# Optimization experiments

Measured on AMD Instinct MI355X. Metric: run time of the kernel, lower is better.

Reference implementation:

```python
import jax, jax.numpy as jnp
import numpy as np

D_MODEL = 1024
B, S = 4, 2048


def setup_inputs() -> dict:
    key = jax.random.key(0)
    kx, km, kq, kk, kv, ko = jax.random.split(key, 6)
    x = jax.random.normal(kx, (B, S, D_MODEL), dtype=jnp.float32)
    mask = jax.random.randint(km, (B, S, S), 0, 2).astype(jnp.bool_)
    # flax Dense default kernel init: lecun_normal-ish; plain scaled normal is fine for a reference
    init_scale = 1.0 / np.sqrt(D_MODEL)
    Wq = jax.random.normal(kq, (D_MODEL, D_MODEL), dtype=jnp.float32) * init_scale
    Wk = jax.random.normal(kk, (D_MODEL, D_MODEL), dtype=jnp.float32) * init_scale
    Wv = jax.random.normal(kv, (D_MODEL, D_MODEL), dtype=jnp.float32) * init_scale
    Wo = jax.random.normal(ko, (D_MODEL, D_MODEL), dtype=jnp.float32) * init_scale
    return {"x": x, "mask": mask, "Wq": Wq, "Wk": Wk, "Wv": Wv, "Wo": Wo}


def reference(x, mask, Wq, Wk, Wv, Wo):
    # QKV projections (use_bias=False)
    q = jnp.einsum('bsd,de->bse', x, Wq)
    k = jnp.einsum('bsd,de->bse', x, Wk)
    v = jnp.einsum('bsd,de->bse', x, Wv)
    scale = jnp.sqrt(jnp.asarray(q.shape[-1], x.dtype)).astype(x.dtype)
    # [B, S, S] attention scores
    attn_scores = jnp.einsum('bqd,bkd->bqk', q, k) / scale
    attn_scores = jnp.where(mask, attn_scores, jnp.asarray(-1e10, x.dtype))
    attn_weights = jax.nn.softmax(attn_scores, axis=-1)
    attn_output = jnp.einsum('bqk,bkd->bqd', attn_weights, v)
    return jnp.einsum('bsd,de->bse', attn_output, Wo)
```

## Files before the change

### kernel.cpp

```cpp
#include <hip/hip_runtime.h>


#define DM 1024
#define SQ 2048
#define NB 4
typedef unsigned short U16;
typedef unsigned long long U64;
typedef short bhalf8 __attribute__((ext_vector_type(8)));
typedef float f32x4 __attribute__((ext_vector_type(4)));

__device__ inline U16 f2bf(float f) {
  unsigned int u = __float_as_uint(f);
  u += 0x7FFFu + ((u >> 16) & 1u);
  return (U16)(u >> 16);
}
__device__ inline float2 bfp2(unsigned int u) {
  float2 r;
  r.x = __uint_as_float(u << 16);
  r.y = __uint_as_float(u & 0xffff0000u);
  return r;
}
__device__ inline unsigned int packbf(float a, float b) {
  return (unsigned int)f2bf(a) | ((unsigned int)f2bf(b) << 16);
}

__device__ __forceinline__ void gload16(const U16* g, const U16* l) {
  unsigned int m0v =
      (unsigned int)__builtin_amdgcn_readfirstlane((int)(unsigned long long)l);
  asm volatile("s_mov_b32 m0, %0\n\t"
               "global_load_lds_dwordx4 %1, off"
               :
               : "s"(m0v), "v"(g)
               : "memory");
}

__global__ __launch_bounds__(256) void conv_f32_bf16(
    const float* __restrict__ src, U16* __restrict__ dst, float* __restrict__ rs) {
  int idx = blockIdx.x * 256 + threadIdx.x;
  if (idx < NB * SQ) rs[idx] = 0.f;
  int i = idx * 8;
  float4 a = *(const float4*)(src + i);
  float4 b = *(const float4*)(src + i + 4);
  uint4 w;
  w.x = packbf(a.x, a.y); w.y = packbf(a.z, a.w);
  w.z = packbf(b.x, b.y); w.w = packbf(b.z, b.w);
  *(uint4*)(dst + i) = w;
}

__global__ __launch_bounds__(256) void pack_mask(
    const int* __restrict__ mask, U64* __restrict__ pm) {
  const int lane = threadIdx.x & 63;
  const int wv = (blockIdx.x * 256 + threadIdx.x) >> 6;
#pragma unroll 4
  for (int i = 0; i < 32; ++i) {
    size_t g = (size_t)wv * 32 + i;
    int mk = mask[g * 64 + lane];
    U64 b = __ballot(mk != 0);
    if (lane == 0) pm[g] = b;
  }
}

__device__ inline void ldcvt16(const float* p, U16* d) {
#pragma unroll
  for (int i = 0; i < 4; ++i) {
    float4 f = *(const float4*)(p + i * 4);
    d[i * 4 + 0] = f2bf(f.x); d[i * 4 + 1] = f2bf(f.y);
    d[i * 4 + 2] = f2bf(f.z); d[i * 4 + 3] = f2bf(f.w);
  }
}
__device__ inline void ldcvt16(const U16* p, U16* d) {
  uint4 a = *(const uint4*)p;
  uint4 b = *(const uint4*)(p + 8);
  *(uint4*)d = a;
  *(uint4*)(d + 8) = b;
}

__global__ __launch_bounds__(256) void transp_w4(
    const float* __restrict__ Wq, const float* __restrict__ Wk,
    const float* __restrict__ Wo, const float* __restrict__ Wv,
    U16* __restrict__ WT, U16* __restrict__ WoT, U16* __restrict__ Wv16) {
  __shared__ U16 tile[64][72];
  const int z = blockIdx.z;
  const int r0 = blockIdx.y * 64, c0 = blockIdx.x * 64;
  const int t = threadIdx.x;
  const int tr = t >> 2, tc = (t & 3) * 16;
  if (z == 3) {
    U16 vals[16];
    ldcvt16(Wv + (size_t)(r0 + tr) * DM + c0 + tc, vals);
    U16* op = Wv16 + (size_t)(r0 + tr) * DM + c0 + tc;
    *(uint4*)op = *(uint4*)&vals[0];
    *(uint4*)(op + 8) = *(uint4*)&vals[8];
    return;
  }
  const float* src = (z == 0) ? Wq : (z == 1) ? Wk : Wo;
  U16* d = (z == 2) ? WoT : WT + (size_t)z * DM * DM;
  ldcvt16(src + (size_t)(r0 + tr) * DM + c0 + tc, &tile[tr][tc]);
  __syncthreads();
  U16 vals[16];
#pragma unroll
  for (int m = 0; m < 16; ++m) vals[m] = tile[tc + m][tr];
  U16* op = d + (size_t)(c0 + tr) * DM + r0 + tc;
  *(uint4*)op = *(uint4*)&vals[0];
  *(uint4*)(op + 8) = *(uint4*)&vals[8];
}

__global__ __launch_bounds__(256) void transp_bf16(
    const U16* __restrict__ src, U16* __restrict__ dst, int R, int C) {
  __shared__ U16 tile[64][72];
  const int z = blockIdx.z;
  src += (size_t)z * R * C;
  dst += (size_t)z * R * C;
  const int r0 = blockIdx.y * 64, c0 = blockIdx.x * 64;
  const int t = threadIdx.x;
  const int tr = t >> 2, tc = (t & 3) * 16;
  ldcvt16(src + (size_t)(r0 + tr) * C + c0 + tc, &tile[tr][tc]);
  __syncthreads();
  U16 vals[16];
#pragma unroll
  for (int m = 0; m < 16; ++m) vals[m] = tile[tc + m][tr];
  U16* op = dst + (size_t)(c0 + tr) * R + r0 + tc;
  *(uint4*)op = *(uint4*)&vals[0];
  *(uint4*)(op + 8) = *(uint4*)&vals[8];
}

template <int EP>
__global__ __launch_bounds__(256) void gemm_mfma(
    const U16* __restrict__ A, const U16* __restrict__ B, void* __restrict__ Cv,
    int M, int N, int K, long long sA, long long sB, long long sC,
    const int* __restrict__ mask, float* __restrict__ rowsum, float scale) {
  __shared__ U16 As[128 * 72];
  __shared__ U16 Bs[128 * 72];
  const int t = threadIdx.x;
  const int lane = t & 63, wave = t >> 6;
  const int wm = wave >> 1, wn = wave & 1;
  const int q = lane >> 4, ln = lane & 15;
  const int z = blockIdx.z;
  const int m0 = blockIdx.y * 128, n0 = blockIdx.x * 128;
  A += (size_t)z * sA;
  B += (size_t)z * sB;

  f32x4 acc[4][4] = {};

  const int srow = t >> 3;
  const int scol = (t & 7) * 8;

  for (int k0 = 0; k0 < K; k0 += 64) {
    const U16* ga = A + (size_t)(m0 + srow) * K + k0 + scol;
    const U16* gb = B + (size_t)(n0 + srow) * K + k0 + scol;
#pragma unroll
    for (int it = 0; it < 4; ++it) {
      uint4 va = *(const uint4*)(ga + (size_t)it * 32 * K);
      uint4 vb = *(const uint4*)(gb + (size_t)it * 32 * K);
      *(uint4*)&As[(it * 32 + srow) * 72 + scol] = va;
      *(uint4*)&Bs[(it * 32 + srow) * 72 + scol] = vb;
    }
    __syncthreads();
#pragma unroll
    for (int kk = 0; kk < 64; kk += 32) {
      bhalf8 af[4], bg[4];
#pragma unroll
      for (int i = 0; i < 4; ++i) {
        af[i] = *(const bhalf8*)&As[(wm * 64 + i * 16 + ln) * 72 + kk + q * 8];
        bg[i] = *(const bhalf8*)&Bs[(wn * 64 + i * 16 + ln) * 72 + kk + q * 8];
      }
#pragma unroll
      for (int i = 0; i < 4; ++i)
#pragma unroll
        for (int j = 0; j < 4; ++j)
          acc[i][j] = __builtin_amdgcn_mfma_f32_16x16x32_bf16(af[i], bg[j], acc[i][j], 0, 0, 0);
    }
    __syncthreads();
  }

#pragma unroll
  for (int i = 0; i < 4; ++i) {
#pragma unroll
    for (int r = 0; r < 4; ++r) {
      const int rr = m0 + wm * 64 + i * 16 + q * 4 + r;
      float linv = 0.f;
      if constexpr (EP == 2) linv = 1.0f / (rowsum[(size_t)z * M + rr] + 1e-30f);
#pragma unroll
      for (int j = 0; j < 4; ++j) {
        const int c = n0 + wn * 64 + j * 16 + ln;
        float v = acc[i][j][r];
        if constexpr (EP == 0) {
          ((U16*)Cv)[(size_t)z * sC + (size_t)rr * N + c] = f2bf(v);
        } else {
          ((float*)Cv)[(size_t)z * sC + (size_t)rr * N + c] = v * linv;
        }
      }
    }
  }
}

template <int EP, int WM>
__global__ __launch_bounds__(512, 1) void gemm8(
    const U16* __restrict__ A, const U16* __restrict__ B, void* __restrict__ Cv,
    int M, int N, int K, long long sA, long long sB, long long sC,
    const U64* __restrict__ pmask, float* __restrict__ rowsum, float scale) {
  constexpr int WN = 8 / WM;
  constexpr int BN = WN * 64;
  constexpr int MR = 256 / WM;
  constexpr int FM = MR / 16;
  constexpr int IMq = FM / 2;
  constexpr int HB = BN / 2;
  constexpr int CB = HB / 64;
  constexpr int VW = 4 + 2 * CB;
  __shared__ __attribute__((aligned(16))) U16 Abuf[2][256 * 64];
  __shared__ __attribute__((aligned(16))) U16 Bbuf[2][BN * 64];
  const int t = threadIdx.x;
  const int lane = t & 63, wave = t >> 6;
  const int wm = wave / WN, wn = wave % WN;
  const int q = lane >> 4, ln = lane & 15;
  const int lxor = ln & 7;

  const int gx = gridDim.x, gy = gridDim.y;
  int lin = blockIdx.x + gx * (blockIdx.y + gy * blockIdx.z);
  const int cpx = (gx * gy * gridDim.z) >> 3;
  lin = (lin & 7) * cpx + (lin >> 3);
  const int bz = lin / (gx * gy);
  const int rem = lin - bz * gx * gy;
  const int by = rem / gx, bx = rem - by * gx;

  const int m0 = by * 256, n0 = bx * BN;
  const U16* Abase = A + (size_t)bz * sA + (size_t)m0 * K;
  const U16* Bbase = B + (size_t)bz * sB + (size_t)n0 * K;

  const int pr = wave * 8 + (lane >> 3);
  const int cchunk = (((lane & 7) ^ ((lane >> 3) & 7)) << 3);
  int la[4];
#pragma unroll
  for (int c = 0; c < 4; ++c) {
    int p = c * 64 + pr;
    int mh = p >> 7, q64 = p & 127;
    la[c] = (q64 / (MR / 2)) * MR + mh * (MR / 2) + (q64 % (MR / 2));
  }
  int lb[4] = {0, 0, 0, 0};
#pragma unroll
  for (int c = 0; c < 2 * CB; ++c) {
    int p = c * 64 + pr;
    int nh = p / HB, rem2 = p % HB;
    lb[c] = (rem2 >> 5) * 64 + nh * 32 + (rem2 & 31);
  }
  const U16* gA0 = Abase + (size_t)la[0] * K + cchunk;
  const U16* gA1 = Abase + (size_t)la[1] * K + cchunk;
  const U16* gA2 = Abase + (size_t)la[2] * K + cchunk;
  const U16* gA3 = Abase + (size_t)la[3] * K + cchunk;
  const U16* gB0 = Bbase + (size_t)lb[0] * K + cchunk;
  const U16* gB1 = (CB == 2) ? Bbase + (size_t)lb[1] * K + cchunk : gB0;
  const U16* gB2 = Bbase + (size_t)lb[CB] * K + cchunk;
  const U16* gB3 = (CB == 2) ? Bbase + (size_t)lb[3] * K + cchunk : gB2;
  const int wofs = wave * 8 * 64;

#define ST_AX(bi, ko) { gload16(gA0 + (ko), &Abuf[bi][0 * 64 + wofs]);         \
                        gload16(gA1 + (ko), &Abuf[bi][64 * 64 + wofs]); }
#define ST_AY(bi, ko) { gload16(gA2 + (ko), &Abuf[bi][128 * 64 + wofs]);       \
                        gload16(gA3 + (ko), &Abuf[bi][192 * 64 + wofs]); }
#define ST_BE(bi, ko) { gload16(gB0 + (ko), &Bbuf[bi][0 * 64 + wofs]);         \
                        if (CB == 2) gload16(gB1 + (ko), &Bbuf[bi][64 * 64 + wofs]); }
#define ST_BO(bi, ko) { gload16(gB2 + (ko), &Bbuf[bi][HB * 64 + wofs]);        \
                        if (CB == 2) gload16(gB3 + (ko), &Bbuf[bi][(HB + 64) * 64 + wofs]); }

  f32x4 acc[FM][4] = {};
  bhalf8 af[IMq][2], bgE[2][2], bgO[2][2];

#define LDA(bi, mh) {                                                          \
  _Pragma("unroll") for (int im = 0; im < IMq; ++im)                           \
  _Pragma("unroll") for (int kx = 0; kx < 2; ++kx)                             \
    af[im][kx] = *(const bhalf8*)&Abuf[bi][                                    \
        ((mh) * 128 + wm * (MR / 2) + im * 16 + ln) * 64 +                     \
        (((kx * 4 + q) ^ lxor) << 3)]; }
#define LDB(bi, nh, BG) {                                                      \
  _Pragma("unroll") for (int jn = 0; jn < 2; ++jn)                             \
  _Pragma("unroll") for (int kx = 0; kx < 2; ++kx)                             \
    BG[jn][kx] = *(const bhalf8*)&Bbuf[bi][                                    \
        ((nh) * HB + wn * 32 + jn * 16 + ln) * 64 +                            \
        (((kx * 4 + q) ^ lxor) << 3)]; }
#define MQ(mh, nh, BG) {                                                       \
  __builtin_amdgcn_s_setprio(1);                                               \
  _Pragma("unroll") for (int im = 0; im < IMq; ++im)                           \
  _Pragma("unroll") for (int jn = 0; jn < 2; ++jn)                             \
  _Pragma("unroll") for (int kx = 0; kx < 2; ++kx)                             \
    acc[(mh) * IMq + im][(nh) * 2 + jn] =                                      \
        __builtin_amdgcn_mfma_f32_16x16x32_bf16(                               \
            af[im][kx], BG[jn][kx], acc[(mh) * IMq + im][(nh) * 2 + jn],       \
            0, 0, 0);                                                          \
  __builtin_amdgcn_s_setprio(0); }
#define WAITV(n) asm volatile("s_waitcnt vmcnt(%0)" :: "i"(n) : "memory")
#define BAR() __builtin_amdgcn_s_barrier()
#define LGKM0() asm volatile("s_waitcnt lgkmcnt(0)" ::: "memory")

#define TILE8(bi, nbi, kA, kB)                                                 \
  {                                                                            \
    ST_BO(nbi, kA); WAITV(VW);                                                 \
    LDA(bi, 0); LDB(bi, 0, bgE);                                               \
    BAR(); LGKM0(); MQ(0, 0, bgE); BAR();                                      \
    ST_AY(nbi, kA); WAITV(VW);                                                 \
    LDB(bi, 1, bgO);                                                           \
    BAR(); LGKM0(); MQ(0, 1, bgO); BAR();                                      \
    ST_AX(bi, kB); WAITV(VW);                                                  \
    LDA(bi, 1);                                                                \
    BAR(); LGKM0(); MQ(1, 0, bgE); BAR();                                      \
    ST_BE(bi, kB); WAITV(VW);                                                  \
    BAR(); LGKM0(); MQ(1, 1, bgO); BAR();                                      \
  }

  const int NT = K >> 6;
  ST_AX(0, 0); ST_BE(0, 0); ST_BO(0, 0); ST_AY(0, 0);
  ST_AX(1, 64); ST_BE(1, 64);
  WAITV(VW); BAR();
  for (int tt = 0; tt < NT; tt += 2) {
    const int k1 = (tt + 1) * 64;
    const int k2 = (tt + 2 < NT) ? (tt + 2) * 64 : 0;
    const int k3 = (tt + 3 < NT) ? (tt + 3) * 64 : 0;
    TILE8(0, 1, k1, k2);
    TILE8(1, 0, k2, k3);
  }
  WAITV(0);

#undef ST_AX
#undef ST_AY
#undef ST_BE
#undef ST_BO
#undef LDA
#undef LDB
#undef MQ
#undef WAITV
#undef BAR
#undef LGKM0
#undef TILE8

#pragma unroll
  for (int i = 0; i < FM; ++i) {
#pragma unroll
    for (int r = 0; r < 4; ++r) {
      const int rr = m0 + wm * MR + i * 16 + q * 4 + r;
      float linv = 0.f;
      if constexpr (EP == 2) linv = 1.0f / (rowsum[(size_t)bz * M + rr] + 1e-30f);
      U64 m64 = 0;
      if constexpr (EP == 1)
        m64 = pmask[((size_t)bz * M + rr) * (N >> 6) + (n0 >> 6) + wn];
      float psum = 0.f;
#pragma unroll
      for (int j = 0; j < 4; ++j) {
        const int c = n0 + wn * 64 + j * 16 + ln;
        float v = acc[i][j][r];
        if constexpr (EP == 0) {
          ((U16*)Cv)[(size_t)bz * sC + (size_t)rr * N + c] = f2bf(v);
        } else if constexpr (EP == 1) {
          int mk = (int)((m64 >> (j * 16 + ln)) & 1ull);
          float p = mk ? __expf(v * scale) : 0.f;
          U16 pb = f2bf(p);
          ((U16*)Cv)[(size_t)bz * sC + (size_t)rr * N + c] = pb;
          psum += __uint_as_float((unsigned int)pb << 16);
        } else {
          ((float*)Cv)[(size_t)bz * sC + (size_t)rr * N + c] = v * linv;
        }
      }
      if constexpr (EP == 1) {
#pragma unroll
        for (int off = 8; off > 0; off >>= 1) psum += __shfl_xor(psum, off, 64);
        if (ln == 0) atomicAdd(&rowsum[(size_t)bz * M + rr], psum);
      }
    }
  }
}

__device__ inline float4 load4(const float* p) { return *(const float4*)p; }
__device__ inline float4 load4(const U16* p) {
  uint2 w = *(const uint2*)p;
  float2 f0 = bfp2(w.x), f1 = bfp2(w.y);
  return make_float4(f0.x, f0.y, f1.x, f1.y);
}
__device__ inline void store4(float* p, float a, float b, float c, float d) {
  *(float4*)p = make_float4(a, b, c, d);
}
__device__ inline void store4(U16* p, float a, float b, float c, float d) {
  uint2 w;
  w.x = packbf(a, b);
  w.y = packbf(c, d);
  *(uint2*)p = w;
}
template <typename TA, typename TB, typename TC>
__global__ __launch_bounds__(256) void gemm_t(
    const TA* __restrict__ A, const TB* __restrict__ B,
    TC* __restrict__ C, int M, int N, int K) {
  __shared__ float As[16][64];
  __shared__ float Bs[16][64];
  const int t = threadIdx.x;
  const int tx = t & 15, ty = t >> 4;
  const int m0 = blockIdx.y * 64;
  const int n0 = blockIdx.x * 64;
  const int arow = t >> 2, akq = (t & 3) * 4;
  const int brow = t >> 4, bcg = (t & 15) * 4;
  float acc[4][4] = {};
  for (int k0 = 0; k0 < K; k0 += 16) {
    {
      float4 f = load4(A + (size_t)(m0 + arow) * K + k0 + akq);
      As[akq + 0][arow] = f.x; As[akq + 1][arow] = f.y;
      As[akq + 2][arow] = f.z; As[akq + 3][arow] = f.w;
    }
    {
      float4 f = load4(B + (size_t)(k0 + brow) * N + n0 + bcg);
      *(float4*)&Bs[brow][bcg] = f;
    }
    __syncthreads();
#pragma unroll
    for (int kk = 0; kk < 16; ++kk) {
      float4 a = *(const float4*)&As[kk][ty * 4];
      float4 b = *(const float4*)&Bs[kk][tx * 4];
      float av[4] = {a.x, a.y, a.z, a.w};
      float bv[4] = {b.x, b.y, b.z, b.w};
#pragma unroll
      for (int i = 0; i < 4; ++i)
#pragma unroll
        for (int j = 0; j < 4; ++j) acc[i][j] += av[i] * bv[j];
    }
    __syncthreads();
  }
#pragma unroll
  for (int i = 0; i < 4; ++i)
    store4(&C[(size_t)(m0 + ty * 4 + i) * N + n0 + tx * 4],
           acc[i][0], acc[i][1], acc[i][2], acc[i][3]);
}
__global__ __launch_bounds__(256) void flash_wave(
    const U16* __restrict__ Q, const U16* __restrict__ Kd,
    const U16* __restrict__ V, const int* __restrict__ mask,
    U16* __restrict__ O) {
  __shared__ float q_s[4][DM];
  const int t = threadIdx.x;
  const int w = t >> 6;
  const int lane = t & 63;
  const int row = blockIdx.x * 4 + w;
  const int b = row >> 11;
  const size_t bo = (size_t)b * SQ * DM;
  const size_t mrow0 = (size_t)row * SQ;
  {
    const U16* qp = Q + (size_t)row * DM + lane * 16;
    uint4 w0 = *(const uint4*)qp;
    uint4 w1 = *(const uint4*)(qp + 8);
    float* dst = &q_s[w][lane * 16];
    float2 f;
    f = bfp2(w0.x); dst[0] = f.x;  dst[1] = f.y;
    f = bfp2(w0.y); dst[2] = f.x;  dst[3] = f.y;
    f = bfp2(w0.z); dst[4] = f.x;  dst[5] = f.y;
    f = bfp2(w0.w); dst[6] = f.x;  dst[7] = f.y;
    f = bfp2(w1.x); dst[8] = f.x;  dst[9] = f.y;
    f = bfp2(w1.y); dst[10] = f.x; dst[11] = f.y;
    f = bfp2(w1.z); dst[12] = f.x; dst[13] = f.y;
    f = bfp2(w1.w); dst[14] = f.x; dst[15] = f.y;
  }
  __syncthreads();
  float m = -3.0e38f, l = 0.f;
  float o[16] = {};
  const int dbase = lane * 16;
  const float* qrow = q_s[w];
  for (int j0 = 0; j0 < SQ; j0 += 64) {
    float s;
    {
      const U16* kp = Kd + bo + (size_t)(j0 + lane) * DM;
      float acc = 0.f;
      for (int d = 0; d < DM; d += 8) {
        uint4 kw = *(const uint4*)(kp + d);
        float2 a0 = bfp2(kw.x), a1 = bfp2(kw.y), a2 = bfp2(kw.z), a3 = bfp2(kw.w);
        acc += qrow[d] * a0.x + qrow[d + 1] * a0.y + qrow[d + 2] * a1.x +
               qrow[d + 3] * a1.y + qrow[d + 4] * a2.x + qrow[d + 5] * a2.y +
               qrow[d + 6] * a3.x + qrow[d + 7] * a3.y;
      }
      s = acc * 0.03125f;
      if (mask[mrow0 + j0 + lane] == 0) s = -1e10f;
    }
    float ms = s;
#pragma unroll
    for (int off = 32; off > 0; off >>= 1) ms = fmaxf(ms, __shfl_xor(ms, off, 64));
    float mn = fmaxf(m, ms);
    float alpha = __expf(m - mn);
    float p = __expf(s - mn);
    float ps = p;
#pragma unroll
    for (int off = 32; off > 0; off >>= 1) ps += __shfl_xor(ps, off, 64);
    l = l * alpha + ps;
    m = mn;
#pragma unroll
    for (int k = 0; k < 16; ++k) o[k] *= alpha;
    const U16* vp = V + bo + (size_t)j0 * DM + dbase;
    for (int j = 0; j < 64; ++j) {
      float pj = __shfl(p, j, 64);
      uint4 v0 = *(const uint4*)(vp + (size_t)j * DM);
      uint4 v1 = *(const uint4*)(vp + (size_t)j * DM + 8);
      float2 f0 = bfp2(v0.x), f1 = bfp2(v0.y), f2 = bfp2(v0.z), f3 = bfp2(v0.w);
      float2 g0 = bfp2(v1.x), g1 = bfp2(v1.y), g2 = bfp2(v1.z), g3 = bfp2(v1.w);
      o[0] += pj * f0.x;  o[1] += pj * f0.y;  o[2] += pj * f1.x;  o[3] += pj * f1.y;
      o[4] += pj * f2.x;  o[5] += pj * f2.y;  o[6] += pj * f3.x;  o[7] += pj * f3.y;
      o[8] += pj * g0.x;  o[9] += pj * g0.y;  o[10] += pj * g1.x; o[11] += pj * g1.y;
      o[12] += pj * g2.x; o[13] += pj * g2.y; o[14] += pj * g3.x; o[15] += pj * g3.y;
    }
  }
  float linv = (l > 0.f) ? (1.0f / l) : 0.f;
  U16* op = O + (size_t)row * DM + dbase;
  uint4 r0, r1;
  r0.x = packbf(o[0] * linv, o[1] * linv);
  r0.y = packbf(o[2] * linv, o[3] * linv);
  r0.z = packbf(o[4] * linv, o[5] * linv);
  r0.w = packbf(o[6] * linv, o[7] * linv);
  r1.x = packbf(o[8] * linv, o[9] * linv);
  r1.y = packbf(o[10] * linv, o[11] * linv);
  r1.z = packbf(o[12] * linv, o[13] * linv);
  r1.w = packbf(o[14] * linv, o[15] * linv);
  *(uint4*)op = r0;
  *(uint4*)(op + 8) = r1;
}

extern "C" void kernel_launch(void* const* d_in, const int* in_sizes, int n_in,
                              void* d_out, int out_size, void* d_ws, size_t ws_size,
                              hipStream_t stream) {
  const float* x  = (const float*)d_in[0];
  const int* mask = (const int*)d_in[1];
  const float* Wq = (const float*)d_in[2];
  const float* Wk = (const float*)d_in[3];
  const float* Wv = (const float*)d_in[4];
  const float* Wo = (const float*)d_in[5];
  float* out = (float*)d_out;

  const size_t MB = 1u << 20;
  const size_t E = (size_t)NB * SQ * DM;
  const size_t WE = (size_t)DM * DM;

  if (ws_size >= 121 * MB) {
    char* ws = (char*)d_ws;
    U16* WT   = (U16*)ws;
    U16* WoT  = (U16*)(ws + 6 * MB);
    U64* pm   = (U64*)(ws + 6 * MB);
    U16* x16  = (U16*)(ws + 8 * MB);
    U16* Q16  = (U16*)(ws + 24 * MB);
    U16* K16  = (U16*)(ws + 40 * MB);
    U16* U16b = (U16*)(ws + 56 * MB);
    U16* Wv16 = (U16*)(ws + 72 * MB);
    U16* UT16 = (U16*)(ws + 72 * MB);
    U16* P16  = (U16*)(ws + 88 * MB);
    float* rs = (float*)(ws + 120 * MB);

    conv_f32_bf16<<<dim3(E / (256 * 8)), 256, 0, stream>>>(x, x16, rs);
    transp_w4<<<dim3(16, 16, 4), 256, 0, stream>>>(Wq, Wk, Wo, Wv, WT, WoT, Wv16);

    gemm_mfma<0><<<dim3(DM / 128, DM / 128, 1), 256, 0, stream>>>(
        WoT, Wv16, WT + 2 * WE, DM, DM, DM, 0, 0, 0, nullptr, nullptr, 0.f);

    pack_mask<<<dim3(2048), 256, 0, stream>>>(mask, pm);

    gemm8<0, 4><<<dim3(DM / 128, (NB * SQ) / 256, 3), 512, 0, stream>>>(
        x16, WT, Q16, NB * SQ, DM, DM,
        0, (long long)WE, (long long)E, nullptr, nullptr, 0.f);

    transp_bf16<<<dim3(DM / 64, SQ / 64, NB), 256, 0, stream>>>(U16b, UT16, SQ, DM);

    gemm8<1, 2><<<dim3(SQ / 256, SQ / 256, NB), 512, 0, stream>>>(
        Q16, K16, P16, SQ, SQ, DM,
        (long long)SQ * DM, (long long)SQ * DM, (long long)SQ * SQ,
        pm, rs, 0.03125f);

    gemm8<2, 4><<<dim3(DM / 128, SQ / 256, NB), 512, 0, stream>>>(
        P16, UT16, out, SQ, DM, SQ,
        (long long)SQ * SQ, (long long)DM * SQ, (long long)SQ * DM,
        nullptr, rs, 0.f);
  } else {
    U16* Kw = (U16*)d_ws;
    U16* Vw = Kw + E;
    U16* Qw = Vw + E;
    U16* Ow = Qw;
    dim3 blk(256);
    dim3 gg(DM / 64, (NB * SQ) / 64);
    gemm_t<float, float, U16><<<gg, blk, 0, stream>>>(x, Wk, Kw, NB * SQ, DM, DM);
    gemm_t<float, float, U16><<<gg, blk, 0, stream>>>(x, Wv, Vw, NB * SQ, DM, DM);
    gemm_t<float, float, U16><<<gg, blk, 0, stream>>>(x, Wq, Qw, NB * SQ, DM, DM);
    flash_wave<<<dim3((NB * SQ) / 4), blk, 0, stream>>>(Qw, Kw, Vw, mask, Ow);
    gemm_t<U16, float, float><<<gg, blk, 0, stream>>>(Ow, Wo, out, NB * SQ, DM, DM);
  }
}
```

Baseline: 324.3 us.

## Add two-phase pipelined GEMM schedule for non-WM==2 configurations

```diff
diff --git a/kernel.cpp b/kernel.cpp
--- a/kernel.cpp
+++ b/kernel.cpp
@@ -262,28 +262,28 @@
                         if (CB == 2) gload16(gB3 + (ko), &Bbuf[bi][(HB + 64) * 64 + wofs]); }
 
   f32x4 acc[FM][4] = {};
-  bhalf8 af[IMq][2], bgE[2][2], bgO[2][2];
-
-#define LDA(bi, mh) {                                                          \
+  bhalf8 afX[IMq][2], afY[IMq][2], bgE[2][2], bgO[2][2];
+
+#define LDA(bi, mh, DST) {                                                     \
   _Pragma("unroll") for (int im = 0; im < IMq; ++im)                           \
   _Pragma("unroll") for (int kx = 0; kx < 2; ++kx)                             \
-    af[im][kx] = *(const bhalf8*)&Abuf[bi][                                    \
+    DST[im][kx] = *(const bhalf8*)&Abuf[bi][                                   \
         ((mh) * 128 + wm * (MR / 2) + im * 16 + ln) * 64 +                     \
         (((kx * 4 + q) ^ lxor) << 3)]; }
-#define LDB(bi, nh, BG) {                                                      \
+#define LDB(bi, nh, DST) {                                                     \
   _Pragma("unroll") for (int jn = 0; jn < 2; ++jn)                             \
   _Pragma("unroll") for (int kx = 0; kx < 2; ++kx)                             \
-    BG[jn][kx] = *(const bhalf8*)&Bbuf[bi][                                    \
+    DST[jn][kx] = *(const bhalf8*)&Bbuf[bi][                                   \
         ((nh) * HB + wn * 32 + jn * 16 + ln) * 64 +                            \
         (((kx * 4 + q) ^ lxor) << 3)]; }
-#define MQ(mh, nh, BG) {                                                       \
+#define MQ(mh, nh, AF, BG) {                                                   \
   __builtin_amdgcn_s_setprio(1);                                               \
   _Pragma("unroll") for (int im = 0; im < IMq; ++im)                           \
   _Pragma("unroll") for (int jn = 0; jn < 2; ++jn)                             \
   _Pragma("unroll") for (int kx = 0; kx < 2; ++kx)                             \
     acc[(mh) * IMq + im][(nh) * 2 + jn] =                                      \
         __builtin_amdgcn_mfma_f32_16x16x32_bf16(                               \
-            af[im][kx], BG[jn][kx], acc[(mh) * IMq + im][(nh) * 2 + jn],       \
+            AF[im][kx], BG[jn][kx], acc[(mh) * IMq + im][(nh) * 2 + jn],       \
             0, 0, 0);                                                          \
   __builtin_amdgcn_s_setprio(0); }
 #define WAITV(n) asm volatile("s_waitcnt vmcnt(%0)" :: "i"(n) : "memory")
@@ -293,28 +293,56 @@
 #define TILE8(bi, nbi, kA, kB)                                                 \
   {                                                                            \
     ST_BO(nbi, kA); WAITV(VW);                                                 \
-    LDA(bi, 0); LDB(bi, 0, bgE);                                               \
-    BAR(); LGKM0(); MQ(0, 0, bgE); BAR();                                      \
+    LDA(bi, 0, afX); LDB(bi, 0, bgE);                                          \
+    BAR(); LGKM0(); MQ(0, 0, afX, bgE); BAR();                                 \
     ST_AY(nbi, kA); WAITV(VW);                                                 \
     LDB(bi, 1, bgO);                                                           \
-    BAR(); LGKM0(); MQ(0, 1, bgO); BAR();                                      \
+    BAR(); LGKM0(); MQ(0, 1, afX, bgO); BAR();                                 \
     ST_AX(bi, kB); WAITV(VW);                                                  \
-    LDA(bi, 1);                                                                \
-    BAR(); LGKM0(); MQ(1, 0, bgE); BAR();                                      \
+    LDA(bi, 1, afX);                                                           \
+    BAR(); LGKM0(); MQ(1, 0, afX, bgE); BAR();                                 \
     ST_BE(bi, kB); WAITV(VW);                                                  \
-    BAR(); LGKM0(); MQ(1, 1, bgO); BAR();                                      \
+    BAR(); LGKM0(); MQ(1, 1, afX, bgO); BAR();                                 \
+  }
+
+#define TILE2(bi, nbi, kA, kB)                                                 \
+  {                                                                            \
+    ST_AY(nbi, kA); WAITV(VW);                                                 \
+    LDA(bi, 0, afX); LDB(bi, 0, bgE); LDB(bi, 1, bgO);                         \
+    BAR(); LGKM0();                                                            \
+    MQ(0, 0, afX, bgE);                                                        \
+    LDA(bi, 1, afY);                                                           \
+    MQ(0, 1, afX, bgO);                                                        \
+    BAR();                                                                     \
+    ST_AX(bi, kB); ST_BE(bi, kB); ST_BO(bi, kB); WAITV(VW);                    \
+    BAR(); LGKM0();                                                            \
+    MQ(1, 0, afY, bgE); MQ(1, 1, afY, bgO);                                    \
+    BAR();                                                                     \
   }
 
   const int NT = K >> 6;
-  ST_AX(0, 0); ST_BE(0, 0); ST_BO(0, 0); ST_AY(0, 0);
-  ST_AX(1, 64); ST_BE(1, 64);
-  WAITV(VW); BAR();
-  for (int tt = 0; tt < NT; tt += 2) {
-    const int k1 = (tt + 1) * 64;
-    const int k2 = (tt + 2 < NT) ? (tt + 2) * 64 : 0;
-    const int k3 = (tt + 3 < NT) ? (tt + 3) * 64 : 0;
-    TILE8(0, 1, k1, k2);
-    TILE8(1, 0, k2, k3);
+  if constexpr (WM == 2) {
+    ST_AX(0, 0); ST_BE(0, 0); ST_BO(0, 0); ST_AY(0, 0);
+    ST_AX(1, 64); ST_BE(1, 64);
+    WAITV(VW); BAR();
+    for (int tt = 0; tt < NT; tt += 2) {
+      const int k1 = (tt + 1) * 64;
+      const int k2 = (tt + 2 < NT) ? (tt + 2) * 64 : 0;
+      const int k3 = (tt + 3 < NT) ? (tt + 3) * 64 : 0;
+      TILE8(0, 1, k1, k2);
+      TILE8(1, 0, k2, k3);
+    }
+  } else {
+    ST_AX(0, 0); ST_BE(0, 0); ST_BO(0, 0); ST_AY(0, 0);
+    ST_AX(1, 64); ST_BE(1, 64); ST_BO(1, 64);
+    WAITV(VW); BAR();
+    for (int tt = 0; tt < NT; tt += 2) {
+      const int k1 = (tt + 1) * 64;
+      const int k2 = (tt + 2 < NT) ? (tt + 2) * 64 : 0;
+      const int k3 = (tt + 3 < NT) ? (tt + 3) * 64 : 0;
+      TILE2(0, 1, k1, k2);
+      TILE2(1, 0, k2, k3);
+    }
   }
   WAITV(0);
 
@@ -329,6 +357,7 @@
 #undef BAR
 #undef LGKM0
 #undef TILE8
+#undef TILE2
 
 #pragma unroll
   for (int i = 0; i < FM; ++i) {
```

New measurement: 332.6 us. 2.6% more time.

## Fold prep, mask packing and V transpose into neighboring kernels as extra blocks

Applied to the files above, without the earlier changes.

```diff
diff --git a/kernel.cpp b/kernel.cpp
--- a/kernel.cpp
+++ b/kernel.cpp
@@ -34,32 +34,6 @@
                : "memory");
 }
 
-__global__ __launch_bounds__(256) void conv_f32_bf16(
-    const float* __restrict__ src, U16* __restrict__ dst, float* __restrict__ rs) {
-  int idx = blockIdx.x * 256 + threadIdx.x;
-  if (idx < NB * SQ) rs[idx] = 0.f;
-  int i = idx * 8;
-  float4 a = *(const float4*)(src + i);
-  float4 b = *(const float4*)(src + i + 4);
-  uint4 w;
-  w.x = packbf(a.x, a.y); w.y = packbf(a.z, a.w);
-  w.z = packbf(b.x, b.y); w.w = packbf(b.z, b.w);
-  *(uint4*)(dst + i) = w;
-}
-
-__global__ __launch_bounds__(256) void pack_mask(
-    const int* __restrict__ mask, U64* __restrict__ pm) {
-  const int lane = threadIdx.x & 63;
-  const int wv = (blockIdx.x * 256 + threadIdx.x) >> 6;
-#pragma unroll 4
-  for (int i = 0; i < 32; ++i) {
-    size_t g = (size_t)wv * 32 + i;
-    int mk = mask[g * 64 + lane];
-    U64 b = __ballot(mk != 0);
-    if (lane == 0) pm[g] = b;
-  }
-}
-
 __device__ inline void ldcvt16(const float* p, U16* d) {
 #pragma unroll
   for (int i = 0; i < 4; ++i) {
@@ -75,14 +49,29 @@
   *(uint4*)(d + 8) = b;
 }
 
-__global__ __launch_bounds__(256) void transp_w4(
+__global__ __launch_bounds__(256) void prep(
+    const float* __restrict__ x, U16* __restrict__ x16, float* __restrict__ rs,
     const float* __restrict__ Wq, const float* __restrict__ Wk,
     const float* __restrict__ Wo, const float* __restrict__ Wv,
     U16* __restrict__ WT, U16* __restrict__ WoT, U16* __restrict__ Wv16) {
   __shared__ U16 tile[64][72];
-  const int z = blockIdx.z;
-  const int r0 = blockIdx.y * 64, c0 = blockIdx.x * 64;
   const int t = threadIdx.x;
+  if (blockIdx.x < 4096) {
+    int idx = blockIdx.x * 256 + t;
+    if (idx < NB * SQ) rs[idx] = 0.f;
+    int i = idx * 8;
+    float4 a = *(const float4*)(x + i);
+    float4 b = *(const float4*)(x + i + 4);
+    uint4 w;
+    w.x = packbf(a.x, a.y); w.y = packbf(a.z, a.w);
+    w.z = packbf(b.x, b.y); w.w = packbf(b.z, b.w);
+    *(uint4*)(x16 + i) = w;
+    return;
+  }
+  const int tw = blockIdx.x - 4096;
+  const int z = tw >> 8;
+  const int rem = tw & 255;
+  const int r0 = (rem >> 4) * 64, c0 = (rem & 15) * 64;
   const int tr = t >> 2, tc = (t & 3) * 16;
   if (z == 3) {
     U16 vals[16];
@@ -100,25 +89,6 @@
 #pragma unroll
   for (int m = 0; m < 16; ++m) vals[m] = tile[tc + m][tr];
   U16* op = d + (size_t)(c0 + tr) * DM + r0 + tc;
-  *(uint4*)op = *(uint4*)&vals[0];
-  *(uint4*)(op + 8) = *(uint4*)&vals[8];
-}
-
-__global__ __launch_bounds__(256) void transp_bf16(
-    const U16* __restrict__ src, U16* __restrict__ dst, int R, int C) {
-  __shared__ U16 tile[64][72];
-  const int z = blockIdx.z;
-  src += (size_t)z * R * C;
-  dst += (size_t)z * R * C;
-  const int r0 = blockIdx.y * 64, c0 = blockIdx.x * 64;
-  const int t = threadIdx.x;
-  const int tr = t >> 2, tc = (t & 3) * 16;
-  ldcvt16(src + (size_t)(r0 + tr) * C + c0 + tc, &tile[tr][tc]);
-  __syncthreads();
-  U16 vals[16];
-#pragma unroll
-  for (int m = 0; m < 16; ++m) vals[m] = tile[tc + m][tr];
-  U16* op = dst + (size_t)(c0 + tr) * R + r0 + tc;
   *(uint4*)op = *(uint4*)&vals[0];
   *(uint4*)(op + 8) = *(uint4*)&vals[8];
 }
@@ -197,7 +167,9 @@
 __global__ __launch_bounds__(512, 1) void gemm8(
     const U16* __restrict__ A, const U16* __restrict__ B, void* __restrict__ Cv,
     int M, int N, int K, long long sA, long long sB, long long sC,
-    const U64* __restrict__ pmask, float* __restrict__ rowsum, float scale) {
+    const U64* __restrict__ pmask, float* __restrict__ rowsum, float scale,
+    int gx, int gy, int gz,
+    const void* __restrict__ taux, void* __restrict__ taux2) {
   constexpr int WN = 8 / WM;
   constexpr int BN = WN * 64;
   constexpr int MR = 256 / WM;
@@ -209,14 +181,52 @@
   __shared__ __attribute__((aligned(16))) U16 Abuf[2][256 * 64];
   __shared__ __attribute__((aligned(16))) U16 Bbuf[2][BN * 64];
   const int t = threadIdx.x;
+  const int nwg = gx * gy * gz;
+
+  if ((int)blockIdx.x >= nwg) {
+    const int tb = (int)blockIdx.x - nwg;
+    if constexpr (EP == 0) {
+      const int lane = t & 63;
+      const int wv = tb * 8 + (t >> 6);
+      const int* msk = (const int*)taux;
+      U64* pmo = (U64*)taux2;
+#pragma unroll 4
+      for (int i = 0; i < 32; ++i) {
+        size_t g = (size_t)wv * 32 + i;
+        U64 bb = __ballot(msk[g * 64 + lane] != 0);
+        if (lane == 0) pmo[g] = bb;
+      }
+    } else if constexpr (EP == 1) {
+      const int half = t >> 8;
+      const int tl = t & 255;
+      const int tid = tb * 2 + half;
+      const int z = tid >> 9;
+      const int rem2 = tid & 511;
+      const int r0 = (rem2 >> 4) * 64;
+      const int c0 = (rem2 & 15) * 64;
+      const U16* src = (const U16*)taux + (size_t)z * SQ * DM;
+      U16* dst = (U16*)taux2 + (size_t)z * SQ * DM;
+      const int tr = tl >> 2, tc = (tl & 3) * 16;
+      U16* tile = &Abuf[0][0] + half * (64 * 72);
+      ldcvt16(src + (size_t)(r0 + tr) * DM + c0 + tc, &tile[tr * 72 + tc]);
+      __syncthreads();
+      U16 vals[16];
+#pragma unroll
+      for (int m = 0; m < 16; ++m) vals[m] = tile[(tc + m) * 72 + tr];
+      U16* op = dst + (size_t)(c0 + tr) * SQ + r0 + tc;
+      *(uint4*)op = *(uint4*)&vals[0];
+      *(uint4*)(op + 8) = *(uint4*)&vals[8];
+    }
+    return;
+  }
+
   const int lane = t & 63, wave = t >> 6;
   const int wm = wave / WN, wn = wave % WN;
   const int q = lane >> 4, ln = lane & 15;
   const int lxor = ln & 7;
 
-  const int gx = gridDim.x, gy = gridDim.y;
-  int lin = blockIdx.x + gx * (blockIdx.y + gy * blockIdx.z);
-  const int cpx = (gx * gy * gridDim.z) >> 3;
+  int lin = blockIdx.x;
+  const int cpx = nwg >> 3;
   lin = (lin & 7) * cpx + (lin >> 3);
   const int bz = lin / (gx * gy);
   const int rem = lin - bz * gx * gy;
@@ -540,29 +550,27 @@
     U16* P16  = (U16*)(ws + 88 * MB);
     float* rs = (float*)(ws + 120 * MB);
 
-    conv_f32_bf16<<<dim3(E / (256 * 8)), 256, 0, stream>>>(x, x16, rs);
-    transp_w4<<<dim3(16, 16, 4), 256, 0, stream>>>(Wq, Wk, Wo, Wv, WT, WoT, Wv16);
+    prep<<<dim3(5120), 256, 0, stream>>>(x, x16, rs, Wq, Wk, Wo, Wv, WT, WoT, Wv16);
 
     gemm_mfma<0><<<dim3(DM / 128, DM / 128, 1), 256, 0, stream>>>(
         WoT, Wv16, WT + 2 * WE, DM, DM, DM, 0, 0, 0, nullptr, nullptr, 0.f);
 
-    pack_mask<<<dim3(2048), 256, 0, stream>>>(mask, pm);
-
-    gemm8<0, 4><<<dim3(DM / 128, (NB * SQ) / 256, 3), 512, 0, stream>>>(
+    gemm8<0, 4><<<dim3(768 + 1024), 512, 0, stream>>>(
         x16, WT, Q16, NB * SQ, DM, DM,
-        0, (long long)WE, (long long)E, nullptr, nullptr, 0.f);
-
-    transp_bf16<<<dim3(DM / 64, SQ / 64, NB), 256, 0, stream>>>(U16b, UT16, SQ, DM);
-
-    gemm8<1, 2><<<dim3(SQ / 256, SQ / 256, NB), 512, 0, stream>>>(
+        0, (long long)WE, (long long)E, nullptr, nullptr, 0.f,
+        DM / 128, (NB * SQ) / 256, 3, mask, pm);
+
+    gemm8<1, 2><<<dim3(256 + 1024), 512, 0, stream>>>(
         Q16, K16, P16, SQ, SQ, DM,
         (long long)SQ * DM, (long long)SQ * DM, (long long)SQ * SQ,
-        pm, rs, 0.03125f);
-
-    gemm8<2, 4><<<dim3(DM / 128, SQ / 256, NB), 512, 0, stream>>>(
+        pm, rs, 0.03125f,
+        SQ / 256, SQ / 256, NB, U16b, UT16);
+
+    gemm8<2, 4><<<dim3(256), 512, 0, stream>>>(
         P16, UT16, out, SQ, DM, SQ,
         (long long)SQ * SQ, (long long)DM * SQ, (long long)SQ * DM,
-        nullptr, rs, 0.f);
+        nullptr, rs, 0.f,
+        DM / 128, SQ / 256, NB, nullptr, nullptr);
   } else {
     U16* Kw = (U16*)d_ws;
     U16* Vw = Kw + E;
```

After: 364.3 us. +12.3%, slower.
